# Kernel optimization log

Hardware: AMD Instinct MI355X
Metric: run time of the kernel (lower is better)

Reference implementation:

```python
import jax, jax.numpy as jnp
import numpy as np

B, D, N_CLASSES = 8192, 128, 50


def setup_inputs() -> dict:
    key = jax.random.key(0)
    k1, k2, k3 = jax.random.split(key, 3)
    anchor = jax.random.normal(k1, (B, D), dtype=jnp.float32)
    target = jax.random.normal(k2, (B, D), dtype=jnp.float32)
    labels = jax.random.randint(k3, (B,), 0, N_CLASSES)
    return {"anchor": anchor, "target": target, "labels": labels}


def reference(anchor, target, labels):
    # Faithful vectorization of QuadrupletLoss.nt_xent_loss.
    # Note: the original hardcodes temperature 0.05 (ignores self.temp).
    TEMP = 0.05
    n = labels.shape[0]
    diff = labels[:, None] != labels[None, :]                      # mask2: [B,B]
    same_off = (labels[:, None] == labels[None, :]) & ~jnp.eye(n, dtype=bool)  # mask

    # d[j, m] = <anchor[j], target[m]> / 0.05
    d = jnp.matmul(anchor, target.T) / TEMP                        # [B,B]
    neg = jnp.where(diff, d, -jnp.inf)
    mx = jax.lax.stop_gradient(jnp.max(neg, axis=1))               # maxdot.detach() per j
    mx = jnp.where(jnp.isfinite(mx), mx, 0.0)
    # s[j] = sum_{m: labels[m]!=labels[j]} exp(d[j,m] - mx[j])  (exp(-inf)=0 masks out)
    s = jnp.sum(jnp.exp(neg - mx[:, None]), axis=1)                # [B]

    # Inner double loop: nds[i] = sum over j with labels[j]!=labels[i] of s[j]
    difff = diff.astype(s.dtype)
    nds = difff @ s                                                # [B]
    negcount = jnp.sum(difff, axis=1)                              # negtivesum

    x = jnp.where(negcount > 0, nds / jnp.where(negcount > 0, negcount, 1.0), nds)
    log_prob = -jnp.log(x + 1e-12)                                 # constant across cols
    mask_sum = jnp.sum(same_off, axis=1)
    # (mask * log_prob).sum(1) / clamp(mask_sum,1) == log_prob where mask_sum>0 else 0
    pos_logits = jnp.where(mask_sum > 0, log_prob, 0.0)
    return -jnp.mean(pos_logits)
```

## Files before the change

kernel.cpp:

```cpp
#include <hip/hip_runtime.h>
#include <float.h>
#include <math.h>

typedef __attribute__((ext_vector_type(8))) short short8;
typedef __attribute__((ext_vector_type(8))) _Float16 half8;
typedef __attribute__((ext_vector_type(4))) float f32x4;

constexpr int B_N  = 8192;
constexpr int D_KK = 128;
constexpr int NCLS = 50;
constexpr int NCHUNK = 16;
constexpr int CCOLS = B_N / NCHUNK;
constexpr int BLK_ROWS = 256;
constexpr int NPBLK = 32;
constexpr float C_SCALE = 28.853900817779268f;
constexpr float MARGIN  = 40.0f;
constexpr float NEG_LOW  = -1.0e5f;
constexpr float NEG_MASK = -1.0e30f;

__device__ __forceinline__ float exp2fast(float x) { return __builtin_amdgcn_exp2f(x); }

__device__ __forceinline__ void async_copy16(void* lds, const void* g) {
    __builtin_amdgcn_global_load_lds((const __attribute__((address_space(1))) unsigned int*)g,
                                     (__attribute__((address_space(3))) unsigned int*)lds,
                                     16, 0, 0);
}

__global__ void prep_kernel(const float* __restrict__ a, const float* __restrict__ b,
                            short* __restrict__ aH, short* __restrict__ bH)
{
    const int NPER = B_N * D_KK / 8;
    int i = blockIdx.x * blockDim.x + threadIdx.x;
    const float* src = (i < NPER) ? a : b;
    short*       dst = (i < NPER) ? aH : bH;
    const float  sc  = (i < NPER) ? C_SCALE : 1.0f;
    int j = (i < NPER) ? i : i - NPER;
    const f32x4* sp = (const f32x4*)(src + (size_t)j * 8);
    f32x4 v0 = sp[0], v1 = sp[1];
    short8 h;
#pragma unroll
    for (int e = 0; e < 4; ++e) {
        h[e]     = __builtin_bit_cast(short, (_Float16)(sc * v0[e]));
        h[e + 4] = __builtin_bit_cast(short, (_Float16)(sc * v1[e]));
    }
    *(short8*)(dst + (size_t)j * 8) = h;
}

__global__ __launch_bounds__(512, 4)
void rowstats_kernel(const short* __restrict__ aH, const short* __restrict__ bH,
                     const int* __restrict__ labels,
                     float* __restrict__ pmx, float* __restrict__ ps)
{
    __shared__ __align__(16) char ring[4][8192];

    const int bid   = blockIdx.x;
    const int chunk = bid & (NCHUNK - 1);
    const int R0    = (bid >> 4) * BLK_ROWS;
    const int C0    = chunk * CCOLS;

    const int tid = threadIdx.x;
    const int wid = tid >> 6, l = tid & 63;
    const int l15 = l & 15, l16 = l >> 4;
    const int wrow = R0 + wid * 32;

    half8 aF[2][4];
#pragma unroll
    for (int mf = 0; mf < 2; ++mf) {
        const int arow = wrow + mf * 16 + l15;
#pragma unroll
        for (int ks = 0; ks < 4; ++ks)
            aF[mf][ks] = __builtin_bit_cast(half8,
                *(const short8*)(aH + (size_t)arow * D_KK + ks * 32 + l16 * 8));
    }

    int labA[8];
#pragma unroll
    for (int mf = 0; mf < 2; ++mf)
#pragma unroll
        for (int r = 0; r < 4; ++r)
            labA[mf * 4 + r] = labels[wrow + mf * 16 + l16 * 4 + r];

    float mx[8], sm[8];
#pragma unroll
    for (int i = 0; i < 8; ++i) { mx[i] = NEG_LOW; sm[i] = 0.0f; }

    const int scol  = tid >> 4;
    const int sg    = (tid & 15) ^ (scol & 7);
    const short* sbase = bH + (size_t)(C0 + scol) * D_KK + sg * 8;
    char* ldsW = &ring[0][0] + wid * 1024;

    const int NT = CCOLS / 32;

#define STAGE(t)  async_copy16(ldsW + (((t) & 3) * 8192), sbase + (size_t)((t) & 15) * 32 * D_KK)

    STAGE(0); STAGE(1); STAGE(2);

    for (int t = 0; t < NT; ++t) {
        asm volatile("s_waitcnt vmcnt(2)" ::: "memory");
        __builtin_amdgcn_s_barrier();
        __builtin_amdgcn_sched_barrier(0);
        STAGE(t + 3);

        const char* rb = &ring[t & 3][0];
        f32x4 acc[2][2];
#pragma unroll
        for (int mf = 0; mf < 2; ++mf)
#pragma unroll
            for (int nf = 0; nf < 2; ++nf) acc[mf][nf] = f32x4{0.f, 0.f, 0.f, 0.f};

#pragma unroll
        for (int ks = 0; ks < 4; ++ks) {
            half8 bF[2];
#pragma unroll
            for (int nf = 0; nf < 2; ++nf) {
                int col  = nf * 16 + l15;
                int slot = (ks * 4 + l16) ^ (col & 7);
                bF[nf] = __builtin_bit_cast(half8,
                    *(const short8*)(rb + col * 256 + slot * 16));
            }
#pragma unroll
            for (int mf = 0; mf < 2; ++mf)
#pragma unroll
                for (int nf = 0; nf < 2; ++nf)
                    acc[mf][nf] = __builtin_amdgcn_mfma_f32_16x16x32_f16(
                        aF[mf][ks], bF[nf], acc[mf][nf], 0, 0, 0);
        }

        const int colB = C0 + t * 32;
        int lB[2];
#pragma unroll
        for (int nf = 0; nf < 2; ++nf) lB[nf] = labels[colB + nf * 16 + l15];

#pragma unroll
        for (int mf = 0; mf < 2; ++mf) {
            float gm = fmaxf(fmaxf(fmaxf(acc[mf][0][0], acc[mf][0][1]),
                                   fmaxf(acc[mf][0][2], acc[mf][0][3])),
                             fmaxf(fmaxf(acc[mf][1][0], acc[mf][1][1]),
                                   fmaxf(acc[mf][1][2], acc[mf][1][3])));
            int sk = 1;
#pragma unroll
            for (int r = 0; r < 4; ++r) sk &= (gm < mx[mf * 4 + r] - MARGIN) ? 1 : 0;
            if (!__all(sk)) {
#pragma unroll
                for (int r = 0; r < 4; ++r) {
                    const int i = mf * 4 + r;
                    float v0 = (lB[0] != labA[i]) ? acc[mf][0][r] : NEG_MASK;
                    float v1 = (lB[1] != labA[i]) ? acc[mf][1][r] : NEG_MASK;
                    float nm = fmaxf(mx[i], fmaxf(v0, v1));
                    float e  = exp2fast(v0 - nm) + exp2fast(v1 - nm);
                    sm[i] = sm[i] * exp2fast(mx[i] - nm) + e;
                    mx[i] = nm;
                }
            }
        }
    }
#undef STAGE

#pragma unroll
    for (int i = 0; i < 8; ++i) {
#pragma unroll
        for (int off = 1; off < 16; off <<= 1) {
            float m2 = __shfl_xor(mx[i], off);
            float s2 = __shfl_xor(sm[i], off);
            float nm = fmaxf(mx[i], m2);
            sm[i] = sm[i] * exp2fast(mx[i] - nm) + s2 * exp2fast(m2 - nm);
            mx[i] = nm;
        }
    }
    if (l15 == 0) {
#pragma unroll
        for (int mf = 0; mf < 2; ++mf)
#pragma unroll
            for (int r = 0; r < 4; ++r) {
                int row = wrow + mf * 16 + l16 * 4 + r;
                pmx[chunk * B_N + row] = mx[mf * 4 + r];
                ps [chunk * B_N + row] = sm[mf * 4 + r];
            }
    }
}

__global__ void classsum_kernel(const float* __restrict__ pmx, const float* __restrict__ ps,
                                const int* __restrict__ labels,
                                float* __restrict__ partSum, unsigned int* __restrict__ partCnt)
{
    __shared__ float        csL[NCLS];
    __shared__ unsigned int ccL[NCLS];
    int t = threadIdx.x;
    if (t < NCLS) { csL[t] = 0.0f; ccL[t] = 0u; }
    __syncthreads();

    int j = blockIdx.x * blockDim.x + t;
    float m = -FLT_MAX, s = 0.0f;
#pragma unroll 4
    for (int c = 0; c < NCHUNK; ++c) {
        float m2 = pmx[(size_t)c * B_N + j];
        float s2 = ps [(size_t)c * B_N + j];
        float nm = fmaxf(m, m2);
        s = s * exp2fast(m - nm) + s2 * exp2fast(m2 - nm);
        m = nm;
    }
    int lab = labels[j];
    atomicAdd(&csL[lab], s);
    atomicAdd(&ccL[lab], 1u);
    __syncthreads();
    if (t < NCLS) {
        partSum[blockIdx.x * NCLS + t] = csL[t];
        partCnt[blockIdx.x * NCLS + t] = ccL[t];
    }
}

__global__ void loss_kernel(const float* __restrict__ partSum,
                            const unsigned int* __restrict__ partCnt,
                            float* __restrict__ out)
{
    int c = threadIdx.x;
    float cs = 0.0f;
    unsigned int cc = 0u;
    if (c < NCLS) {
#pragma unroll 4
        for (int b = 0; b < NPBLK; ++b) {
            cs += partSum[b * NCLS + c];
            cc += partCnt[b * NCLS + c];
        }
    }

    float tot = cs;
#pragma unroll
    for (int off = 1; off < 64; off <<= 1) tot += __shfl_xor(tot, off);

    float contrib = 0.0f;
    if (c < NCLS && cc > 0u) {
        float negc = (float)(B_N - (int)cc);
        float nds  = tot - cs;
        float x    = (negc > 0.0f) ? (nds / negc) : nds;
        float lp   = (cc >= 2u) ? (-logf(x + 1e-12f)) : 0.0f;
        contrib = (float)cc * lp;
    }
#pragma unroll
    for (int off = 1; off < 64; off <<= 1) contrib += __shfl_xor(contrib, off);
    if (c == 0) out[0] = -(contrib / (float)B_N);
}

extern "C" void kernel_launch(void* const* d_in, const int* in_sizes, int n_in,
                              void* d_out, int out_size, void* d_ws, size_t ws_size,
                              hipStream_t stream)
{
    const float* anchor = (const float*)d_in[0];
    const float* target = (const float*)d_in[1];
    const int*   labels = (const int*)d_in[2];
    float* out = (float*)d_out;

    const size_t PLANE = (size_t)B_N * D_KK * sizeof(short);
    char* ws = (char*)d_ws;
    short* aH = (short*)(ws + 0 * PLANE);
    short* bH = (short*)(ws + 1 * PLANE);
    float* ps  = (float*)(ws + 2 * PLANE);
    float* pmx = (float*)(ws + 2 * PLANE + sizeof(float) * NCHUNK * B_N);
    char*  cls = ws + 2 * PLANE + 2 * sizeof(float) * NCHUNK * B_N;
    float*        partSum = (float*)cls;
    unsigned int* partCnt = (unsigned int*)(cls + NPBLK * NCLS * sizeof(float));

    prep_kernel<<<2 * (B_N * D_KK / 8) / 256, 256, 0, stream>>>(anchor, target, aH, bH);
    rowstats_kernel<<<(B_N / BLK_ROWS) * NCHUNK, 512, 0, stream>>>(aH, bH, labels, pmx, ps);
    classsum_kernel<<<B_N / 256, 256, 0, stream>>>(pmx, ps, labels, partSum, partCnt);
    loss_kernel<<<1, 64, 0, stream>>>(partSum, partCnt, out);
}
```

Before: 53.90 us.

## Retile rowstats into 128x128 output tiles with single-shot LDS load

The row-statistics kernel changes from 256-row blocks that stream 512 columns through a 4-deep LDS ring into a 64x64 grid of 128x128 tiles. Each tile loads both operands into 64KB of LDS once, then runs a 2x2 wave layout with 4x4 MFMA fragments per wave and a single-pass masked max/exp-sum. The skip-by-margin shortcut is dropped. Partial results go to 64 column chunks instead of 16, so the classsum kernel now reads four times more partials, using a two-pass max then weighted sum. This trades streaming pipelining for more blocks and more register reuse, at the cost of more global partial traffic, lower occupancy from the large LDS footprint, and no overlap of loads with compute within a block.

```diff
diff --git a/kernel.cpp b/kernel.cpp
--- a/kernel.cpp
+++ b/kernel.cpp
@@ -7,19 +7,18 @@
 typedef __attribute__((ext_vector_type(4))) float f32x4;
 
 constexpr int B_N  = 8192;
-constexpr int D_KK = 128;
+constexpr int D_K  = 128;
 constexpr int NCLS = 50;
-constexpr int NCHUNK = 16;
-constexpr int CCOLS = B_N / NCHUNK;
-constexpr int BLK_ROWS = 256;
+constexpr int NCHK = 64;
 constexpr int NPBLK = 32;
-constexpr float C_SCALE = 28.853900817779268f;
-constexpr float MARGIN  = 40.0f;
+constexpr float C_SCALE  = 28.853900817779268f;
 constexpr float NEG_LOW  = -1.0e5f;
 constexpr float NEG_MASK = -1.0e30f;
 
 __device__ __forceinline__ float exp2fast(float x) { return __builtin_amdgcn_exp2f(x); }
-
+__device__ __forceinline__ f32x4 mfma16(half8 a, half8 b, f32x4 c) {
+    return __builtin_amdgcn_mfma_f32_16x16x32_f16(a, b, c, 0, 0, 0);
+}
 __device__ __forceinline__ void async_copy16(void* lds, const void* g) {
     __builtin_amdgcn_global_load_lds((const __attribute__((address_space(1))) unsigned int*)g,
                                      (__attribute__((address_space(3))) unsigned int*)lds,
@@ -29,7 +28,7 @@
 __global__ void prep_kernel(const float* __restrict__ a, const float* __restrict__ b,
                             short* __restrict__ aH, short* __restrict__ bH)
 {
-    const int NPER = B_N * D_KK / 8;
+    const int NPER = B_N * D_K / 8;
     int i = blockIdx.x * blockDim.x + threadIdx.x;
     const float* src = (i < NPER) ? a : b;
     short*       dst = (i < NPER) ? aH : bH;
@@ -46,136 +45,131 @@
     *(short8*)(dst + (size_t)j * 8) = h;
 }
 
-__global__ __launch_bounds__(512, 4)
+__global__ __launch_bounds__(256)
 void rowstats_kernel(const short* __restrict__ aH, const short* __restrict__ bH,
                      const int* __restrict__ labels,
                      float* __restrict__ pmx, float* __restrict__ ps)
 {
-    __shared__ __align__(16) char ring[4][8192];
-
-    const int bid   = blockIdx.x;
-    const int chunk = bid & (NCHUNK - 1);
-    const int R0    = (bid >> 4) * BLK_ROWS;
-    const int C0    = chunk * CCOLS;
+    __shared__ __align__(16) char smem[65536];
+
+    const int bid    = blockIdx.x;
+    const int colblk = bid & 63;
+    const int R0     = (bid >> 6) * 128;
+    const int C0     = colblk * 128;
 
     const int tid = threadIdx.x;
     const int wid = tid >> 6, l = tid & 63;
     const int l15 = l & 15, l16 = l >> 4;
-    const int wrow = R0 + wid * 32;
-
-    half8 aF[2][4];
-#pragma unroll
-    for (int mf = 0; mf < 2; ++mf) {
-        const int arow = wrow + mf * 16 + l15;
-#pragma unroll
-        for (int ks = 0; ks < 4; ++ks)
-            aF[mf][ks] = __builtin_bit_cast(half8,
-                *(const short8*)(aH + (size_t)arow * D_KK + ks * 32 + l16 * 8));
-    }
-
-    int labA[8];
-#pragma unroll
-    for (int mf = 0; mf < 2; ++mf)
-#pragma unroll
-        for (int r = 0; r < 4; ++r)
-            labA[mf * 4 + r] = labels[wrow + mf * 16 + l16 * 4 + r];
-
-    float mx[8], sm[8];
-#pragma unroll
-    for (int i = 0; i < 8; ++i) { mx[i] = NEG_LOW; sm[i] = 0.0f; }
-
-    const int scol  = tid >> 4;
-    const int sg    = (tid & 15) ^ (scol & 7);
-    const short* sbase = bH + (size_t)(C0 + scol) * D_KK + sg * 8;
-    char* ldsW = &ring[0][0] + wid * 1024;
-
-    const int NT = CCOLS / 32;
-
-#define STAGE(t)  async_copy16(ldsW + (((t) & 3) * 8192), sbase + (size_t)((t) & 15) * 32 * D_KK)
-
-    STAGE(0); STAGE(1); STAGE(2);
-
-    for (int t = 0; t < NT; ++t) {
-        asm volatile("s_waitcnt vmcnt(2)" ::: "memory");
-        __builtin_amdgcn_s_barrier();
-        __builtin_amdgcn_sched_barrier(0);
-        STAGE(t + 3);
-
-        const char* rb = &ring[t & 3][0];
-        f32x4 acc[2][2];
-#pragma unroll
-        for (int mf = 0; mf < 2; ++mf)
-#pragma unroll
-            for (int nf = 0; nf < 2; ++nf) acc[mf][nf] = f32x4{0.f, 0.f, 0.f, 0.f};
-
-#pragma unroll
-        for (int ks = 0; ks < 4; ++ks) {
-            half8 bF[2];
-#pragma unroll
-            for (int nf = 0; nf < 2; ++nf) {
-                int col  = nf * 16 + l15;
-                int slot = (ks * 4 + l16) ^ (col & 7);
-                bF[nf] = __builtin_bit_cast(half8,
-                    *(const short8*)(rb + col * 256 + slot * 16));
+    const int wr = wid >> 1, wc = wid & 1;
+
+    int labA[4];
+#pragma unroll
+    for (int mf = 0; mf < 4; ++mf)
+        labA[mf] = labels[R0 + wr * 64 + mf * 16 + l15];
+    int lb[4][4];
+#pragma unroll
+    for (int nf = 0; nf < 4; ++nf) {
+        int4 t4 = *(const int4*)(labels + C0 + wc * 64 + nf * 16 + l16 * 4);
+        lb[nf][0] = t4.x; lb[nf][1] = t4.y; lb[nf][2] = t4.z; lb[nf][3] = t4.w;
+    }
+
+    {
+        const int srow = tid >> 4;
+        const int sp   = tid & 15;
+#pragma unroll
+        for (int is = 0; is < 8; ++is) {
+            int row = is * 16 + srow;
+            int gs  = sp ^ (row & 7);
+            char* da = smem + is * 4096 + (wid << 10);
+            async_copy16(da,         aH + (size_t)(R0 + row) * D_K + gs * 8);
+            async_copy16(da + 32768, bH + (size_t)(C0 + row) * D_K + gs * 8);
+        }
+    }
+    __syncthreads();
+
+    f32x4 acc[4][4];
+#pragma unroll
+    for (int mf = 0; mf < 4; ++mf)
+#pragma unroll
+        for (int nf = 0; nf < 4; ++nf) acc[mf][nf] = f32x4{0.f, 0.f, 0.f, 0.f};
+
+    const int swz = l15 & 7;
+#pragma unroll
+    for (int ks = 0; ks < 4; ++ks) {
+        const int g = (ks * 4 + l16) ^ swz;
+        half8 af[4], bf[4];
+#pragma unroll
+        for (int mf = 0; mf < 4; ++mf) {
+            int row = wr * 64 + mf * 16 + l15;
+            af[mf] = *(const half8*)(smem + row * 256 + g * 16);
+        }
+#pragma unroll
+        for (int nf = 0; nf < 4; ++nf) {
+            int row = wc * 64 + nf * 16 + l15;
+            bf[nf] = *(const half8*)(smem + 32768 + row * 256 + g * 16);
+        }
+#pragma unroll
+        for (int mf = 0; mf < 4; ++mf)
+#pragma unroll
+            for (int nf = 0; nf < 4; ++nf)
+                acc[mf][nf] = mfma16(bf[nf], af[mf], acc[mf][nf]);
+    }
+
+    float fm[4], fs[4];
+#pragma unroll
+    for (int mf = 0; mf < 4; ++mf) {
+        const int la = labA[mf];
+        float v[16];
+        float m = NEG_LOW;
+#pragma unroll
+        for (int nf = 0; nf < 4; ++nf)
+#pragma unroll
+            for (int r = 0; r < 4; ++r) {
+                float x = (lb[nf][r] != la) ? acc[mf][nf][r] : NEG_MASK;
+                v[nf * 4 + r] = x;
+                m = fmaxf(m, x);
             }
-#pragma unroll
-            for (int mf = 0; mf < 2; ++mf)
-#pragma unroll
-                for (int nf = 0; nf < 2; ++nf)
-                    acc[mf][nf] = __builtin_amdgcn_mfma_f32_16x16x32_f16(
-                        aF[mf][ks], bF[nf], acc[mf][nf], 0, 0, 0);
-        }
-
-        const int colB = C0 + t * 32;
-        int lB[2];
-#pragma unroll
-        for (int nf = 0; nf < 2; ++nf) lB[nf] = labels[colB + nf * 16 + l15];
-
-#pragma unroll
-        for (int mf = 0; mf < 2; ++mf) {
-            float gm = fmaxf(fmaxf(fmaxf(acc[mf][0][0], acc[mf][0][1]),
-                                   fmaxf(acc[mf][0][2], acc[mf][0][3])),
-                             fmaxf(fmaxf(acc[mf][1][0], acc[mf][1][1]),
-                                   fmaxf(acc[mf][1][2], acc[mf][1][3])));
-            int sk = 1;
-#pragma unroll
-            for (int r = 0; r < 4; ++r) sk &= (gm < mx[mf * 4 + r] - MARGIN) ? 1 : 0;
-            if (!__all(sk)) {
-#pragma unroll
-                for (int r = 0; r < 4; ++r) {
-                    const int i = mf * 4 + r;
-                    float v0 = (lB[0] != labA[i]) ? acc[mf][0][r] : NEG_MASK;
-                    float v1 = (lB[1] != labA[i]) ? acc[mf][1][r] : NEG_MASK;
-                    float nm = fmaxf(mx[i], fmaxf(v0, v1));
-                    float e  = exp2fast(v0 - nm) + exp2fast(v1 - nm);
-                    sm[i] = sm[i] * exp2fast(mx[i] - nm) + e;
-                    mx[i] = nm;
-                }
-            }
-        }
-    }
-#undef STAGE
-
-#pragma unroll
-    for (int i = 0; i < 8; ++i) {
-#pragma unroll
-        for (int off = 1; off < 16; off <<= 1) {
-            float m2 = __shfl_xor(mx[i], off);
-            float s2 = __shfl_xor(sm[i], off);
-            float nm = fmaxf(mx[i], m2);
-            sm[i] = sm[i] * exp2fast(mx[i] - nm) + s2 * exp2fast(m2 - nm);
-            mx[i] = nm;
-        }
-    }
-    if (l15 == 0) {
-#pragma unroll
-        for (int mf = 0; mf < 2; ++mf)
-#pragma unroll
-            for (int r = 0; r < 4; ++r) {
-                int row = wrow + mf * 16 + l16 * 4 + r;
-                pmx[chunk * B_N + row] = mx[mf * 4 + r];
-                ps [chunk * B_N + row] = sm[mf * 4 + r];
-            }
+        float s0 = 0.f, s1 = 0.f, s2 = 0.f, s3 = 0.f;
+#pragma unroll
+        for (int k = 0; k < 4; ++k) {
+            s0 += exp2fast(v[k]      - m);
+            s1 += exp2fast(v[k + 4]  - m);
+            s2 += exp2fast(v[k + 8]  - m);
+            s3 += exp2fast(v[k + 12] - m);
+        }
+        float s = (s0 + s1) + (s2 + s3);
+#pragma unroll
+        for (int off = 16; off < 64; off <<= 1) {
+            float m2 = __shfl_xor(m, off);
+            float sx = __shfl_xor(s, off);
+            float nm = fmaxf(m, m2);
+            s = s * exp2fast(m - nm) + sx * exp2fast(m2 - nm);
+            m = nm;
+        }
+        fm[mf] = m; fs[mf] = s;
+    }
+
+    __syncthreads();
+    float* mb = (float*)smem;
+    if (wc == 1 && l < 16) {
+#pragma unroll
+        for (int mf = 0; mf < 4; ++mf) {
+            int rl = wr * 64 + mf * 16 + l15;
+            mb[rl * 2]     = fm[mf];
+            mb[rl * 2 + 1] = fs[mf];
+        }
+    }
+    __syncthreads();
+    if (wc == 0 && l < 16) {
+#pragma unroll
+        for (int mf = 0; mf < 4; ++mf) {
+            int rl = wr * 64 + mf * 16 + l15;
+            float m2 = mb[rl * 2], s2 = mb[rl * 2 + 1];
+            float nm = fmaxf(fm[mf], m2);
+            float s  = fs[mf] * exp2fast(fm[mf] - nm) + s2 * exp2fast(m2 - nm);
+            pmx[(size_t)colblk * B_N + R0 + rl] = nm;
+            ps [(size_t)colblk * B_N + R0 + rl] = s;
+        }
     }
 }
 
@@ -190,15 +184,14 @@
     __syncthreads();
 
     int j = blockIdx.x * blockDim.x + t;
-    float m = -FLT_MAX, s = 0.0f;
-#pragma unroll 4
-    for (int c = 0; c < NCHUNK; ++c) {
-        float m2 = pmx[(size_t)c * B_N + j];
-        float s2 = ps [(size_t)c * B_N + j];
-        float nm = fmaxf(m, m2);
-        s = s * exp2fast(m - nm) + s2 * exp2fast(m2 - nm);
-        m = nm;
-    }
+    float m = -FLT_MAX;
+#pragma unroll 8
+    for (int c = 0; c < NCHK; ++c) m = fmaxf(m, pmx[(size_t)c * B_N + j]);
+    float s = 0.0f;
+#pragma unroll 8
+    for (int c = 0; c < NCHK; ++c)
+        s += ps[(size_t)c * B_N + j] * exp2fast(pmx[(size_t)c * B_N + j] - m);
+
     int lab = labels[j];
     atomicAdd(&csL[lab], s);
     atomicAdd(&ccL[lab], 1u);
@@ -250,18 +243,19 @@
     const int*   labels = (const int*)d_in[2];
     float* out = (float*)d_out;
 
-    const size_t PLANE = (size_t)B_N * D_KK * sizeof(short);
+    const size_t PLANE = (size_t)B_N * D_K * sizeof(short);
+    const size_t PART  = (size_t)NCHK * B_N * sizeof(float);
     char* ws = (char*)d_ws;
-    short* aH = (short*)(ws + 0 * PLANE);
-    short* bH = (short*)(ws + 1 * PLANE);
-    float* ps  = (float*)(ws + 2 * PLANE);
-    float* pmx = (float*)(ws + 2 * PLANE + sizeof(float) * NCHUNK * B_N);
-    char*  cls = ws + 2 * PLANE + 2 * sizeof(float) * NCHUNK * B_N;
+    short* aH = (short*)(ws);
+    short* bH = (short*)(ws + PLANE);
+    float* pmx = (float*)(ws + 2 * PLANE);
+    float* ps  = (float*)(ws + 2 * PLANE + PART);
+    char*  cls = ws + 2 * PLANE + 2 * PART;
     float*        partSum = (float*)cls;
     unsigned int* partCnt = (unsigned int*)(cls + NPBLK * NCLS * sizeof(float));
 
-    prep_kernel<<<2 * (B_N * D_KK / 8) / 256, 256, 0, stream>>>(anchor, target, aH, bH);
-    rowstats_kernel<<<(B_N / BLK_ROWS) * NCHUNK, 512, 0, stream>>>(aH, bH, labels, pmx, ps);
+    prep_kernel<<<2 * (B_N * D_K / 8) / 256, 256, 0, stream>>>(anchor, target, aH, bH);
+    rowstats_kernel<<<64 * 64, 256, 0, stream>>>(aH, bH, labels, pmx, ps);
     classsum_kernel<<<B_N / 256, 256, 0, stream>>>(pmx, ps, labels, partSum, partCnt);
     loss_kernel<<<1, 64, 0, stream>>>(partSum, partCnt, out);
 }
```

Measured after the change: 64.52 us. 19.7% more time.
